# Optimization experiments

Hardware: AMD Instinct MI355X
Metric: run time of the kernel (lower is better)

Reference implementation:

```python
import jax, jax.numpy as jnp
import numpy as np

B, N, FEAT, HID, OUT = 128, 64, 4, 256, 4
E = N * (N - 1)  # fully-connected graph, no self-loops


def _onehot_rel():
    # off-diagonal (recv, send) pairs, matching NRI's encode_onehot construction
    recv, send = np.where(~np.eye(N, dtype=bool))
    rel_rec = np.eye(N, dtype=np.float32)[recv]   # [E, N]
    rel_send = np.eye(N, dtype=np.float32)[send]  # [E, N]
    return jnp.asarray(rel_rec), jnp.asarray(rel_send)


def setup_inputs() -> dict:
    key = jax.random.key(0)
    ks = jax.random.split(key, 8)
    rel_rec, rel_send = _onehot_rel()

    def xavier(k, shape):
        fan_in, fan_out = shape
        lim = (6.0 / (fan_in + fan_out)) ** 0.5
        return jax.random.uniform(k, shape, jnp.float32, -lim, lim)

    return {
        "inputs": jax.random.normal(ks[0], (B, N, FEAT), jnp.float32),
        "edges": jax.random.normal(ks[1], (B, E, 2), jnp.float32),  # unused by forward (as in source)
        "rel_rec": rel_rec,
        "rel_send": rel_send,
        "W_msg1": xavier(ks[2], (2 * FEAT, HID)), "b_msg1": jnp.zeros((HID,), jnp.float32),
        "W_msg2": xavier(ks[3], (HID, HID)),      "b_msg2": jnp.zeros((HID,), jnp.float32),
        "W_out1": xavier(ks[4], (FEAT + HID, HID)), "b_out1": jnp.zeros((HID,), jnp.float32),
        "W_out2": xavier(ks[5], (HID, HID)),      "b_out2": jnp.zeros((HID,), jnp.float32),
        "W_out3": xavier(ks[6], (HID, OUT)),      "b_out3": jnp.zeros((OUT,), jnp.float32),
    }


def reference(inputs, edges, rel_rec, rel_send,
              W_msg1, b_msg1, W_msg2, b_msg2,
              W_out1, b_out1, W_out2, b_out2, W_out3, b_out3):
    x = inputs.reshape(inputs.shape[0], inputs.shape[1], -1)  # [B, N, F]
    # gather node features to edges via one-hot matmuls (faithful to source)
    receivers = jnp.einsum('en,bnf->bef', rel_rec, x)   # [B, E, F]
    senders = jnp.einsum('en,bnf->bef', rel_send, x)    # [B, E, F]
    pre_msg = jnp.concatenate([receivers, senders], axis=-1)  # [B, E, 2F]
    # edge MLP (dropout_prob = 0.0 -> identity)
    msg = jax.nn.relu(pre_msg @ W_msg1 + b_msg1)
    msg = jax.nn.relu(msg @ W_msg2 + b_msg2)            # [B, E, HID]
    # scatter-aggregate back to nodes via rel_rec^T
    agg_msg = jnp.einsum('en,beh->bnh', rel_rec, msg)   # [B, N, HID]
    out = jnp.concatenate([x, agg_msg], axis=-1)        # [B, N, F+HID]
    out = jax.nn.relu(out @ W_out1 + b_out1)
    out = jax.nn.relu(out @ W_out2 + b_out2)
    out = out @ W_out3 + b_out3                          # [B, N, 4]
    return out
```

## Files before the change

kernel.cpp:

```cpp
#include <hip/hip_runtime.h>
#include <cstddef>

typedef _Float16 f16_t;
typedef _Float16 f16x8 __attribute__((ext_vector_type(8)));
typedef float    f32x4  __attribute__((ext_vector_type(4)));
typedef float    f32x16 __attribute__((ext_vector_type(16)));

static constexpr int NN = 64;
static constexpr int FF = 4;
static constexpr int HH = 256;


__device__ inline void pack_frag16(const float* __restrict__ src, f16_t* __restrict__ dst,
                                   int fid, int ksteps, int mode)
{
    if (fid >= ksteps * 1024) return;
    int lane = fid & 63;
    int nt   = (fid >> 6) & 15;
    int ks   = fid >> 10;
    int col  = nt * 16 + (lane & 15);
    int kb   = ks * 32 + (lane >> 4) * 8;
    #pragma unroll
    for (int j = 0; j < 8; ++j) {
        int k = kb + j;
        float v;
        if (mode == 0) {
            v = src[k * 256 + col];
        } else {
            if (k < 256)      v = src[(4 + k) * 256 + col];
            else if (k < 260) v = src[(k - 256) * 256 + col];
            else              v = 0.f;
        }
        dst[(size_t)fid * 8 + j] = (f16_t)v;
    }
}

__device__ inline void pack_frag32(const float* __restrict__ src, f16_t* __restrict__ dst,
                                   int fid)
{
    int lane = fid & 63;
    int nt   = (fid >> 6) & 7;
    int ks   = fid >> 9;
    int col  = nt * 32 + (lane & 31);
    int kb   = ks * 16 + (lane >> 5) * 8;
    #pragma unroll
    for (int j = 0; j < 8; ++j)
        dst[(size_t)fid * 8 + j] = (f16_t)src[(kb + j) * 256 + col];
}

__global__ void prep_all(const float* __restrict__ x,
                         const float* __restrict__ W_msg1,
                         const float* __restrict__ W_msg2,
                         const float* __restrict__ W_out1,
                         const float* __restrict__ W_out2,
                         f16_t* __restrict__ W2p, f16_t* __restrict__ W1op,
                         f16_t* __restrict__ W2op, f16_t* __restrict__ Vp)
{
    int bid = blockIdx.x, tid = threadIdx.x;
    if (bid < 32) {
        pack_frag32(W_msg2, W2p, bid * 256 + tid);
    } else if (bid < 68) {
        pack_frag16(W_out1, W1op, (bid - 32) * 256 + tid, 9, 1);
    } else if (bid < 100) {
        pack_frag16(W_out2, W2op, (bid - 68) * 256 + tid, 8, 0);
    } else {
        int gid  = (bid - 100) * 256 + tid;
        int rown = gid >> 5;
        int h0   = (gid & 31) * 8;
        float4 xv = ((const float4*)x)[rown];
        f16x8 o;
        #pragma unroll
        for (int u = 0; u < 8; ++u) {
            float s = xv.x * W_msg1[4 * HH + h0 + u] + xv.y * W_msg1[5 * HH + h0 + u]
                    + xv.z * W_msg1[6 * HH + h0 + u] + xv.w * W_msg1[7 * HH + h0 + u];
            o[u] = (f16_t)s;
        }
        *(f16x8*)(Vp + (size_t)rown * HH + h0) = o;
    }
}

__global__ __launch_bounds__(512, 4) void edge_kernel(
    const float* __restrict__ x,
    const float* __restrict__ W1,
    const float* __restrict__ b1,
    const f16_t* __restrict__ Vp,
    const f16_t* __restrict__ W2p,
    const float* __restrict__ b2,
    f16_t* __restrict__ innode)
{
    __shared__ __align__(16) char h1[128 * 512];
    __shared__ __align__(16) f16_t Utab[2][256];

    const int tid  = threadIdx.x;
    const int lane = tid & 63;
    const int w    = tid >> 6;
    const int b    = blockIdx.x >> 5;
    const int pr   = blockIdx.x & 31;
    const int i0   = pr * 2, i1 = i0 + 1;

    {
        int rs   = tid >> 8;
        int h    = tid & 255;
        int node = rs ? i1 : i0;
        const float* xr = x + (b * NN + node) * FF;
        float s = b1[h] + xr[0] * W1[h] + xr[1] * W1[HH + h]
                        + xr[2] * W1[2 * HH + h] + xr[3] * W1[3 * HH + h];
        Utab[rs][h] = (f16_t)s;
    }
    if (tid < 64) {
        int node = (tid < 32) ? i0 : i1;
        int c = tid & 31;
        float v = (c < 4) ? x[(b * NN + node) * FF + c] : 0.f;
        innode[(size_t)(b * NN + node) * 288 + 256 + c] = (f16_t)v;
    }
    __syncthreads();

    {
        const int hb = tid & 31;
        const int rg = tid >> 5;
        const int h0 = hb * 8;
        const int recv = (rg < 8) ? i0 : i1;
        const f16x8 fz = {};
        f16x8 u8 = *(const f16x8*)&Utab[rg >> 3][h0];
        const int j0 = (rg & 7) * 8;
        const f16x8* vrow = (const f16x8*)(Vp + (size_t)(b * NN + j0) * HH + h0);
        #pragma unroll
        for (int k = 0; k < 8; ++k) {
            int r = rg * 8 + k;
            f16x8 v8 = vrow[k * (HH / 8)];
            f16x8 hv = __builtin_elementwise_max(u8 + v8, fz);
            *(f16x8*)(h1 + r * 512 + (((hb ^ (r & 31)) & 31) << 4)) = hv;
        }
        if ((rg & 7) == (recv >> 3)) {
            int k = recv & 7;
            int r = rg * 8 + k;
            *(f16x8*)(h1 + r * 512 + (((hb ^ (r & 31)) & 31) << 4)) = fz;
        }
    }
    __syncthreads();

    const int ln = lane & 31;
    const int kh = lane >> 5;
    const int wm = w >> 2;
    const int wn = w & 3;

    float b2v[2];
    #pragma unroll
    for (int nt = 0; nt < 2; ++nt) b2v[nt] = b2[(wn * 2 + nt) * 32 + ln];

    f32x16 acc[2][2];
    #pragma unroll
    for (int mt = 0; mt < 2; ++mt)
        #pragma unroll
        for (int nt = 0; nt < 2; ++nt)
            #pragma unroll
            for (int e = 0; e < 16; ++e) acc[mt][nt][e] = b2v[nt];

    #pragma unroll
    for (int ks = 0; ks < 16; ++ks) {
        f16x8 bb[2];
        #pragma unroll
        for (int nt = 0; nt < 2; ++nt)
            bb[nt] = *(const f16x8*)(W2p + (size_t)((ks * 8 + wn * 2 + nt) * 64 + lane) * 8);
        #pragma unroll
        for (int mt = 0; mt < 2; ++mt) {
            int row = wm * 64 + mt * 32 + ln;
            int c16 = (ks * 2 + kh) ^ (row & 31);
            f16x8 a = *(const f16x8*)(h1 + row * 512 + (c16 << 4));
            #pragma unroll
            for (int nt = 0; nt < 2; ++nt)
                acc[mt][nt] = __builtin_amdgcn_mfma_f32_32x32x16_f16(a, bb[nt], acc[mt][nt], 0, 0, 0);
        }
    }

    const int recv = (wm == 0) ? i0 : i1;
    float s[2] = {0.f, 0.f};
    #pragma unroll
    for (int mt = 0; mt < 2; ++mt)
        #pragma unroll
        for (int nt = 0; nt < 2; ++nt) {
            float t = 0.f;
            #pragma unroll
            for (int e = 0; e < 16; ++e) t += fmaxf(acc[mt][nt][e], 0.f);
            s[nt] += t;
        }
    #pragma unroll
    for (int nt = 0; nt < 2; ++nt) s[nt] += __shfl_xor(s[nt], 32);
    if (lane < 32) {
        #pragma unroll
        for (int nt = 0; nt < 2; ++nt) {
            int col = (wn * 2 + nt) * 32 + ln;
            innode[(size_t)(b * NN + recv) * 288 + col] =
                (f16_t)(s[nt] - fmaxf(b2v[nt], 0.f));
        }
    }
}

__global__ __launch_bounds__(256, 4) void node_kernel(
    const f16_t* __restrict__ innode,
    const f16_t* __restrict__ W1op,
    const float* __restrict__ bo1,
    const f16_t* __restrict__ W2op,
    const float* __restrict__ bo2,
    const float* __restrict__ W3,
    const float* __restrict__ bo3,
    float* __restrict__ out)
{
    __shared__ __align__(16) char bufA[16 * 640];
    __shared__ __align__(16) char bufB[16 * 512];
    __shared__ __align__(16) char bufC[16 * 528];

    const int tid  = threadIdx.x;
    const int lane = tid & 63;
    const int w    = tid >> 6;
    const int m0   = blockIdx.x * 16;
    const int lm   = lane & 15, lk = lane >> 4;

    for (int idx = tid; idx < 16 * 36; idx += 256) {
        int r = idx / 36, c = idx - r * 36;
        f16x8 v = *(const f16x8*)(innode + (size_t)(m0 + r) * 288 + c * 8);
        *(f16x8*)(bufA + ((r * 640 + c * 16) ^ ((r & 7) << 4))) = v;
    }
    __syncthreads();

    f32x4 acc1[4];
    #pragma unroll
    for (int nt = 0; nt < 4; ++nt) {
        float bias = bo1[(w * 4 + nt) * 16 + lm];
        acc1[nt] = (f32x4){bias, bias, bias, bias};
    }
    #pragma unroll
    for (int ks = 0; ks < 9; ++ks) {
        f16x8 a = *(const f16x8*)(bufA + ((lm * 640 + ks * 64 + lk * 16) ^ ((lm & 7) << 4)));
        #pragma unroll
        for (int nt = 0; nt < 4; ++nt) {
            f16x8 bb = *(const f16x8*)(W1op + (size_t)((ks * 16 + w * 4 + nt) * 64 + lane) * 8);
            acc1[nt] = __builtin_amdgcn_mfma_f32_16x16x32_f16(a, bb, acc1[nt], 0, 0, 0);
        }
    }
    #pragma unroll
    for (int nt = 0; nt < 4; ++nt) {
        int col = (w * 4 + nt) * 16 + lm;
        #pragma unroll
        for (int j = 0; j < 4; ++j) {
            int row = lk * 4 + j;
            float v = fmaxf(acc1[nt][j], 0.f);
            *(f16_t*)(bufB + ((row * 512 + col * 2) ^ ((row & 7) << 4))) = (f16_t)v;
        }
    }
    __syncthreads();

    f32x4 acc2[4];
    #pragma unroll
    for (int nt = 0; nt < 4; ++nt) {
        float bias = bo2[(w * 4 + nt) * 16 + lm];
        acc2[nt] = (f32x4){bias, bias, bias, bias};
    }
    #pragma unroll
    for (int ks = 0; ks < 8; ++ks) {
        f16x8 a = *(const f16x8*)(bufB + ((lm * 512 + ks * 64 + lk * 16) ^ ((lm & 7) << 4)));
        #pragma unroll
        for (int nt = 0; nt < 4; ++nt) {
            f16x8 bb = *(const f16x8*)(W2op + (size_t)((ks * 16 + w * 4 + nt) * 64 + lane) * 8);
            acc2[nt] = __builtin_amdgcn_mfma_f32_16x16x32_f16(a, bb, acc2[nt], 0, 0, 0);
        }
    }
    f16_t* c16 = (f16_t*)bufC;
    #pragma unroll
    for (int nt = 0; nt < 4; ++nt) {
        int col = (w * 4 + nt) * 16 + lm;
        #pragma unroll
        for (int j = 0; j < 4; ++j) {
            int row = lk * 4 + j;
            float v = fmaxf(acc2[nt][j], 0.f);
            c16[row * 264 + col] = (f16_t)v;
        }
    }
    __syncthreads();

    {
        int m = tid >> 4;
        int o = (tid >> 2) & 3;
        int q = tid & 3;
        const f16_t* crow = c16 + m * 264 + q * 64;
        float s = 0.f;
        int rot = (lane & 15) * 4;
        #pragma unroll 8
        for (int k = 0; k < 64; ++k) {
            int kk = (k + rot) & 63;
            s += (float)crow[kk] * W3[(q * 64 + kk) * 4 + o];
        }
        s += __shfl_xor(s, 1);
        s += __shfl_xor(s, 2);
        if (q == 0) out[(size_t)(m0 + m) * 4 + o] = s + bo3[o];
    }
}

extern "C" void kernel_launch(void* const* d_in, const int* in_sizes, int n_in,
                              void* d_out, int out_size, void* d_ws, size_t ws_size,
                              hipStream_t stream)
{
    (void)in_sizes; (void)n_in; (void)out_size; (void)ws_size;
    const float* x      = (const float*)d_in[0];
    const float* W_msg1 = (const float*)d_in[4];
    const float* b_msg1 = (const float*)d_in[5];
    const float* W_msg2 = (const float*)d_in[6];
    const float* b_msg2 = (const float*)d_in[7];
    const float* W_out1 = (const float*)d_in[8];
    const float* b_out1 = (const float*)d_in[9];
    const float* W_out2 = (const float*)d_in[10];
    const float* b_out2 = (const float*)d_in[11];
    const float* W_out3 = (const float*)d_in[12];
    const float* b_out3 = (const float*)d_in[13];
    float* out = (float*)d_out;

    char* ws = (char*)d_ws;
    f16_t* W2p    = (f16_t*)(ws + 0);
    f16_t* W1op   = (f16_t*)(ws + 131072);
    f16_t* W2op   = (f16_t*)(ws + 278528);
    f16_t* innode = (f16_t*)(ws + 409600);
    f16_t* Vp     = (f16_t*)(ws + 5128192);

    prep_all<<<1124, 256, 0, stream>>>(x, W_msg1, W_msg2, W_out1, W_out2,
                                       W2p, W1op, W2op, Vp);
    edge_kernel<<<4096, 512, 0, stream>>>(x, W_msg1, b_msg1, Vp, W2p, b_msg2, innode);
    node_kernel<<<512, 256, 0, stream>>>(innode, W1op, b_out1, W2op, b_out2,
                                         W_out3, b_out3, out);
}
```

Before: 106.0 us.

## Halve edge kernel block to 4 waves, each covering all 128 rows

The edge kernel now runs 256 threads (4 waves) per block instead of 512. Each wave computes all 128 edge rows (4 M-tiles) for its 64 output columns, so every W2 fragment loaded from global is reused across twice as many MFMA tiles. Each wave also writes both receiver nodes' aggregates. In exchange, each wave holds twice the accumulator registers and there are fewer waves per block, which may lower occupancy and the ability to hide latency. LDS per block is unchanged at 64KB, which limits how many blocks fit per CU.

```diff
diff --git a/kernel.cpp b/kernel.cpp
--- a/kernel.cpp
+++ b/kernel.cpp
@@ -79,7 +79,7 @@
     }
 }
 
-__global__ __launch_bounds__(512, 4) void edge_kernel(
+__global__ __launch_bounds__(256, 2) void edge_kernel(
     const float* __restrict__ x,
     const float* __restrict__ W1,
     const float* __restrict__ b1,
@@ -98,9 +98,11 @@
     const int pr   = blockIdx.x & 31;
     const int i0   = pr * 2, i1 = i0 + 1;
 
-    {
-        int rs   = tid >> 8;
-        int h    = tid & 255;
+    #pragma unroll
+    for (int i = 0; i < 2; ++i) {
+        int e    = tid + i * 256;
+        int rs   = e >> 8;
+        int h    = e & 255;
         int node = rs ? i1 : i0;
         const float* xr = x + (b * NN + node) * FF;
         float s = b1[h] + xr[0] * W1[h] + xr[1] * W1[HH + h]
@@ -119,21 +121,20 @@
         const int hb = tid & 31;
         const int rg = tid >> 5;
         const int h0 = hb * 8;
-        const int recv = (rg < 8) ? i0 : i1;
+        const int recv = (rg < 4) ? i0 : i1;
         const f16x8 fz = {};
-        f16x8 u8 = *(const f16x8*)&Utab[rg >> 3][h0];
-        const int j0 = (rg & 7) * 8;
+        f16x8 u8 = *(const f16x8*)&Utab[rg >> 2][h0];
+        const int j0 = (rg & 3) * 16;
         const f16x8* vrow = (const f16x8*)(Vp + (size_t)(b * NN + j0) * HH + h0);
         #pragma unroll
-        for (int k = 0; k < 8; ++k) {
-            int r = rg * 8 + k;
+        for (int k = 0; k < 16; ++k) {
+            int r = rg * 16 + k;
             f16x8 v8 = vrow[k * (HH / 8)];
             f16x8 hv = __builtin_elementwise_max(u8 + v8, fz);
             *(f16x8*)(h1 + r * 512 + (((hb ^ (r & 31)) & 31) << 4)) = hv;
         }
-        if ((rg & 7) == (recv >> 3)) {
-            int k = recv & 7;
-            int r = rg * 8 + k;
+        if ((rg & 3) == (recv >> 4)) {
+            int r = rg * 16 + (recv & 15);
             *(f16x8*)(h1 + r * 512 + (((hb ^ (r & 31)) & 31) << 4)) = fz;
         }
     }
@@ -141,16 +142,15 @@
 
     const int ln = lane & 31;
     const int kh = lane >> 5;
-    const int wm = w >> 2;
-    const int wn = w & 3;
+    const int wn = w;
 
     float b2v[2];
     #pragma unroll
     for (int nt = 0; nt < 2; ++nt) b2v[nt] = b2[(wn * 2 + nt) * 32 + ln];
 
-    f32x16 acc[2][2];
-    #pragma unroll
-    for (int mt = 0; mt < 2; ++mt)
+    f32x16 acc[4][2];
+    #pragma unroll
+    for (int mt = 0; mt < 4; ++mt)
         #pragma unroll
         for (int nt = 0; nt < 2; ++nt)
             #pragma unroll
@@ -163,8 +163,8 @@
         for (int nt = 0; nt < 2; ++nt)
             bb[nt] = *(const f16x8*)(W2p + (size_t)((ks * 8 + wn * 2 + nt) * 64 + lane) * 8);
         #pragma unroll
-        for (int mt = 0; mt < 2; ++mt) {
-            int row = wm * 64 + mt * 32 + ln;
+        for (int mt = 0; mt < 4; ++mt) {
+            int row = mt * 32 + ln;
             int c16 = (ks * 2 + kh) ^ (row & 31);
             f16x8 a = *(const f16x8*)(h1 + row * 512 + (c16 << 4));
             #pragma unroll
@@ -173,25 +173,28 @@
         }
     }
 
-    const int recv = (wm == 0) ? i0 : i1;
-    float s[2] = {0.f, 0.f};
-    #pragma unroll
-    for (int mt = 0; mt < 2; ++mt)
+    float s0[2] = {0.f, 0.f}, s1[2] = {0.f, 0.f};
+    #pragma unroll
+    for (int mt = 0; mt < 4; ++mt)
         #pragma unroll
         for (int nt = 0; nt < 2; ++nt) {
             float t = 0.f;
             #pragma unroll
             for (int e = 0; e < 16; ++e) t += fmaxf(acc[mt][nt][e], 0.f);
-            s[nt] += t;
-        }
-    #pragma unroll
-    for (int nt = 0; nt < 2; ++nt) s[nt] += __shfl_xor(s[nt], 32);
+            if (mt < 2) s0[nt] += t; else s1[nt] += t;
+        }
+    #pragma unroll
+    for (int nt = 0; nt < 2; ++nt) {
+        s0[nt] += __shfl_xor(s0[nt], 32);
+        s1[nt] += __shfl_xor(s1[nt], 32);
+    }
     if (lane < 32) {
         #pragma unroll
         for (int nt = 0; nt < 2; ++nt) {
+            float sub = fmaxf(b2v[nt], 0.f);
             int col = (wn * 2 + nt) * 32 + ln;
-            innode[(size_t)(b * NN + recv) * 288 + col] =
-                (f16_t)(s[nt] - fmaxf(b2v[nt], 0.f));
+            innode[(size_t)(b * NN + i0) * 288 + col] = (f16_t)(s0[nt] - sub);
+            innode[(size_t)(b * NN + i1) * 288 + col] = (f16_t)(s1[nt] - sub);
         }
     }
 }
@@ -323,7 +326,7 @@
 
     prep_all<<<1124, 256, 0, stream>>>(x, W_msg1, W_msg2, W_out1, W_out2,
                                        W2p, W1op, W2op, Vp);
-    edge_kernel<<<4096, 512, 0, stream>>>(x, W_msg1, b_msg1, Vp, W2p, b_msg2, innode);
+    edge_kernel<<<4096, 256, 0, stream>>>(x, W_msg1, b_msg1, Vp, W2p, b_msg2, innode);
     node_kernel<<<512, 256, 0, stream>>>(innode, W1op, b_out1, W2op, b_out2,
                                          W_out3, b_out3, out);
 }
```

New measurement: 95.59 us. -9.9%, faster.
